# Performance work log

Measured on AMD Instinct MI355X. Metric: run time of the kernel, lower is better.

The kernel has to match this reference:

```python
import jax, jax.numpy as jnp
import numpy as np

PH, PW = 7, 7          # pooled output size (fixed by offset shape in module)
SPP = 2                # sample_per_part: bilinear samples per bin edge
SS = 0.0625            # spatial_scale = 1/16
TRANS_STD = 0.1


def setup_inputs() -> dict:
    key = jax.random.key(0)
    k1, k2, k3, k4, k5 = jax.random.split(key, 5)
    B, C, H, W = 8, 256, 168, 168
    N = 512
    img = W / SS  # input-image extent = 2688
    features = jax.random.normal(k1, (B, C, H, W), dtype=jnp.float32)
    bidx = jax.random.randint(k2, (N,), 0, B).astype(jnp.float32)
    xs = jnp.sort(jax.random.uniform(k3, (N, 2), minval=0.0, maxval=img - 1.0), axis=1)
    ys = jnp.sort(jax.random.uniform(k4, (N, 2), minval=0.0, maxval=img - 1.0), axis=1)
    rois = jnp.stack([bidx, xs[:, 0], ys[:, 0],
                      jnp.minimum(xs[:, 1] + 16.0, img - 1.0),
                      jnp.minimum(ys[:, 1] + 16.0, img - 1.0)], axis=1)
    offset = jax.random.normal(k5, (N, 2, PH, PW), dtype=jnp.float32)
    return {"features": features, "rois": rois, "offset": offset}


def _deform_roi_pool(features, rois, offset):
    B, C, H, W = features.shape
    off = offset * TRANS_STD  # module scales offsets by trans_std
    bidx = jax.lax.stop_gradient(rois[:, 0]).astype(jnp.int32)
    x1, y1, x2, y2 = rois[:, 1], rois[:, 2], rois[:, 3], rois[:, 4]
    # DCN kernel ROI geometry (0.5-pixel aligned, min size 0.1)
    sw = x1 * SS - 0.5
    sh = y1 * SS - 0.5
    rw = jnp.maximum((x2 + 1.0) * SS - 0.5 - sw, 0.1)
    rh = jnp.maximum((y2 + 1.0) * SS - 0.5 - sh, 0.1)
    bin_w, bin_h = rw / PW, rh / PH
    sub_w, sub_h = bin_w / SPP, bin_h / SPP

    e5 = lambda v: v[:, None, None, None, None]  # [N] -> [N,1,1,1,1]
    pw = jnp.arange(PW, dtype=features.dtype).reshape(1, 1, PW, 1, 1)
    ph = jnp.arange(PH, dtype=features.dtype).reshape(1, PH, 1, 1, 1)
    iw = (jnp.arange(SPP, dtype=features.dtype) + 0.5).reshape(1, 1, 1, 1, SPP)
    ih = (jnp.arange(SPP, dtype=features.dtype) + 0.5).reshape(1, 1, 1, SPP, 1)
    offx = off[:, 0][:, :, :, None, None]  # [N,PH,PW,1,1]
    offy = off[:, 1][:, :, :, None, None]

    # sample coords [N,PH,PW,SPP,SPP]: bin start + per-bin learned shift + sub-sample
    x = e5(sw) + pw * e5(bin_w) + offx * e5(rw) + iw * e5(sub_w)
    y = e5(sh) + ph * e5(bin_h) + offy * e5(rh) + ih * e5(sub_h)

    valid = (x > -0.5) & (x < W - 0.5) & (y > -0.5) & (y < H - 0.5)
    xc = jnp.clip(x, 0.0, W - 1.0)
    yc = jnp.clip(y, 0.0, H - 1.0)
    x0f, y0f = jnp.floor(xc), jnp.floor(yc)
    lx, ly = xc - x0f, yc - y0f
    x0 = x0f.astype(jnp.int32)
    y0 = y0f.astype(jnp.int32)
    x1i = jnp.minimum(x0 + 1, W - 1)
    y1i = jnp.minimum(y0 + 1, H - 1)

    # flat gather over (batch, h, w), channels vectorized
    featf = jnp.transpose(features, (0, 2, 3, 1)).reshape(B * H * W, C)
    base = e5(bidx) * (H * W)
    g = lambda yy, xx: featf[base + yy * W + xx]  # [N,PH,PW,SPP,SPP,C]

    w00 = ((1 - ly) * (1 - lx))[..., None]
    w01 = ((1 - ly) * lx)[..., None]
    w10 = (ly * (1 - lx))[..., None]
    w11 = (ly * lx)[..., None]
    val = w00 * g(y0, x0) + w01 * g(y0, x1i) + w10 * g(y1i, x0) + w11 * g(y1i, x1i)
    val = jnp.where(valid[..., None], val, 0.0)

    s = val.sum(axis=(3, 4))                                   # [N,PH,PW,C]
    cnt = valid.sum(axis=(3, 4)).astype(features.dtype)[..., None]
    out = jnp.where(cnt > 0, s / jnp.maximum(cnt, 1.0), 0.0)
    return jnp.transpose(out, (0, 3, 1, 2))                    # [N,C,PH,PW]


def reference(features, rois, offset):
    return _deform_roi_pool(features, rois, offset)
```

## Files before the change

kernel.cpp:

```cpp
#include <hip/hip_runtime.h>
#include <hip/hip_fp16.h>


#define PH_ 7
#define PW_ 7
#define SPP_ 2
#define SS_ 0.0625f
#define TRANS_STD_ 0.1f
#define B_ 8
#define C_ 256
#define H_ 168
#define W_ 168
#define N_ 512
#define HW_ (H_ * W_)
#define HW4_ (HW_ / 4)
#define BINS_ (PH_ * PW_)
#define NSUB_ (SPP_ * SPP_)
#define BLK_ 1024
#define RPC_ 20

#define WS_LIST_OFF_  B_
#define WS_DESC_OFF_I (B_ + B_ * N_)
#define DESC_FLOATS_  (N_ * NSUB_ * BINS_ * 4)
#define WS_NEEDED_    ((size_t)(WS_DESC_OFF_I) * 4 + (size_t)DESC_FLOATS_ * 4)

__global__ __launch_bounds__(512) void build_roi_lists(
    const float* __restrict__ rois, int* __restrict__ ws)
{
    const int r = threadIdx.x;
    if (r < B_) ws[r] = 0;
    __syncthreads();
    const int b = (int)rois[r * 5 + 0];
    const int pos = atomicAdd(&ws[b], 1);
    ws[WS_LIST_OFF_ + b * N_ + pos] = r;
}

__global__ __launch_bounds__(64) void build_desc(
    const float* __restrict__ rois,
    const float* __restrict__ offset,
    float4* __restrict__ desc)
{
    const int r   = blockIdx.x;
    const int bin = threadIdx.x;
    if (bin >= BINS_) return;
    const int ph = bin / PW_;
    const int pw = bin - ph * PW_;

    const float x1r = rois[r * 5 + 1];
    const float y1r = rois[r * 5 + 2];
    const float x2r = rois[r * 5 + 3];
    const float y2r = rois[r * 5 + 4];

    const float sw    = x1r * SS_ - 0.5f;
    const float sh    = y1r * SS_ - 0.5f;
    const float rw    = fmaxf((x2r + 1.0f) * SS_ - 0.5f - sw, 0.1f);
    const float rh    = fmaxf((y2r + 1.0f) * SS_ - 0.5f - sh, 0.1f);
    const float bin_w = rw * (1.0f / PW_);
    const float bin_h = rh * (1.0f / PH_);
    const float sub_w = bin_w * (1.0f / SPP_);
    const float sub_h = bin_h * (1.0f / SPP_);

    const float offx = offset[((r * 2 + 0) * PH_ + ph) * PW_ + pw] * TRANS_STD_;
    const float offy = offset[((r * 2 + 1) * PH_ + ph) * PW_ + pw] * TRANS_STD_;

    const float bx = sw + (float)pw * bin_w + offx * rw;
    const float by = sh + (float)ph * bin_h + offy * rh;

    unsigned pack[NSUB_];
    float lxs[NSUB_], lys[NSUB_];
    int   vals[NSUB_];
    int   cnt = 0;
#pragma unroll
    for (int s = 0; s < NSUB_; ++s) {
        const int ihs = s >> 1;
        const int iws = s & 1;
        const float x = bx + ((float)iws + 0.5f) * sub_w;
        const float y = by + ((float)ihs + 0.5f) * sub_h;
        const int valid = (x > -0.5f) && (x < (float)W_ - 0.5f) &&
                          (y > -0.5f) && (y < (float)H_ - 0.5f);
        const float xc = fminf(fmaxf(x, 0.0f), (float)(W_ - 1));
        const float yc = fminf(fmaxf(y, 0.0f), (float)(H_ - 1));
        const float x0f = floorf(xc);
        const float y0f = floorf(yc);
        const int x0 = (int)x0f;
        const int y0 = (int)y0f;
        const int dx = (x0 + 1 <= W_ - 1) ? 1 : 0;
        const int dy = (y0 + 1 <= H_ - 1) ? 1 : 0;
        pack[s] = (unsigned)(y0 * W_ + x0) | ((unsigned)dx << 15) |
                  ((unsigned)dy << 16);
        lxs[s] = xc - x0f;
        lys[s] = yc - y0f;
        vals[s] = valid;
        cnt += valid;
    }
    const float inv = (cnt > 0) ? (1.0f / (float)cnt) : 0.0f;
#pragma unroll
    for (int s = 0; s < NSUB_; ++s) {
        float4 d;
        d.x = __uint_as_float(pack[s]);
        d.y = lxs[s];
        d.z = lys[s];
        d.w = vals[s] ? inv : 0.0f;
        desc[((size_t)r * NSUB_ + s) * BINS_ + bin] = d;
    }
}

__global__ __launch_bounds__(BLK_, 8) void droi_pool_lds(
    const float* __restrict__ features,
    float* __restrict__ out,
    const int* __restrict__ ws)
{
    __shared__ __half plane[HW_];

    const int c   = blockIdx.x;
    const int b   = blockIdx.y;
    const int tid = threadIdx.x;

    const float4* __restrict__ f4 =
        reinterpret_cast<const float4*>(features + (size_t)(b * C_ + c) * HW_);
    for (int i = tid; i < HW4_; i += BLK_) {
        const float4 v = f4[i];
        union { __half2 h[2]; float2 f2; } u;
        u.h[0].x = __float2half(v.x); u.h[0].y = __float2half(v.y);
        u.h[1].x = __float2half(v.z); u.h[1].y = __float2half(v.w);
        *reinterpret_cast<float2*>(&plane[i * 4]) = u.f2;
    }
    __syncthreads();

    const int cnt_b = ws[b];
    const int* __restrict__ list = ws + WS_LIST_OFF_ + b * N_;
    const float4* __restrict__ desc =
        reinterpret_cast<const float4*>(ws + WS_DESC_OFF_I);

    const int q   = tid / BINS_;
    const int bin = tid - q * BINS_;
    const bool lane_ok = (q < RPC_);

    for (int base = 0; base < cnt_b; base += RPC_) {
        const int idx     = base + q;
        const bool active = lane_ok && (idx < cnt_b);
        const int r = list[active ? idx : 0];

        float acc = 0.0f;
#pragma unroll
        for (int s = 0; s < NSUB_; ++s) {
            const float4 d = desc[((size_t)r * NSUB_ + s) * BINS_ + bin];
            const unsigned pk = __float_as_uint(d.x);
            const int a00 = (int)(pk & 0x7FFFu);
            const int dx  = (int)((pk >> 15) & 1u);
            const int a10 = a00 + (int)((pk >> 16) & 1u) * W_;
            const float lx = d.y;
            const float ly = d.z;

            const float f00 = __half2float(plane[a00]);
            const float f01 = __half2float(plane[a00 + dx]);
            const float f10 = __half2float(plane[a10]);
            const float f11 = __half2float(plane[a10 + dx]);

            const float top = f00 + lx * (f01 - f00);
            const float bot = f10 + lx * (f11 - f10);
            acc += d.w * (top + ly * (bot - top));
        }

        if (active) {
            out[((size_t)r * C_ + c) * BINS_ + bin] = acc;
        }
    }
}

__global__ __launch_bounds__(64) void droi_pool_fallback(
    const float* __restrict__ features,
    const float* __restrict__ rois,
    const float* __restrict__ offset,
    float* __restrict__ out)
{
    const int blk  = blockIdx.x;
    const int n    = blk >> 8;
    const int c    = blk & 255;
    const int lane = threadIdx.x;
    if (lane >= BINS_) return;
    const int ph = lane / PW_;
    const int pw = lane % PW_;

    const float r0  = rois[n * 5 + 0];
    const float x1r = rois[n * 5 + 1];
    const float y1r = rois[n * 5 + 2];
    const float x2r = rois[n * 5 + 3];
    const float y2r = rois[n * 5 + 4];
    const int   b   = (int)r0;

    const float sw    = x1r * SS_ - 0.5f;
    const float sh    = y1r * SS_ - 0.5f;
    const float rw    = fmaxf((x2r + 1.0f) * SS_ - 0.5f - sw, 0.1f);
    const float rh    = fmaxf((y2r + 1.0f) * SS_ - 0.5f - sh, 0.1f);
    const float bin_w = rw / PW_;
    const float bin_h = rh / PH_;
    const float sub_w = bin_w / SPP_;
    const float sub_h = bin_h / SPP_;

    const float offx = offset[((n * 2 + 0) * PH_ + ph) * PW_ + pw] * TRANS_STD_;
    const float offy = offset[((n * 2 + 1) * PH_ + ph) * PW_ + pw] * TRANS_STD_;

    const float bx = sw + (float)pw * bin_w + offx * rw;
    const float by = sh + (float)ph * bin_h + offy * rh;

    const float* __restrict__ f =
        features + (size_t)(b * C_ + c) * (size_t)HW_;

    float s = 0.0f;
    int cnt = 0;
#pragma unroll
    for (int ihs = 0; ihs < SPP_; ++ihs) {
#pragma unroll
        for (int iws = 0; iws < SPP_; ++iws) {
            const float x = bx + ((float)iws + 0.5f) * sub_w;
            const float y = by + ((float)ihs + 0.5f) * sub_h;
            const bool valid = (x > -0.5f) && (x < (float)W_ - 0.5f) &&
                               (y > -0.5f) && (y < (float)H_ - 0.5f);
            const float xc = fminf(fmaxf(x, 0.0f), (float)(W_ - 1));
            const float yc = fminf(fmaxf(y, 0.0f), (float)(H_ - 1));
            const float x0f = floorf(xc);
            const float y0f = floorf(yc);
            const float lx = xc - x0f;
            const float ly = yc - y0f;
            const int x0 = (int)x0f;
            const int y0 = (int)y0f;
            const int x1i = min(x0 + 1, W_ - 1);
            const int y1i = min(y0 + 1, H_ - 1);
            const float f00 = f[y0  * W_ + x0 ];
            const float f01 = f[y0  * W_ + x1i];
            const float f10 = f[y1i * W_ + x0 ];
            const float f11 = f[y1i * W_ + x1i];
            const float v = (1.0f - ly) * (1.0f - lx) * f00 +
                            (1.0f - ly) * lx          * f01 +
                            ly          * (1.0f - lx) * f10 +
                            ly          * lx          * f11;
            if (valid) { s += v; cnt += 1; }
        }
    }
    const float res = (cnt > 0) ? (s / (float)cnt) : 0.0f;
    out[(size_t)(n * C_ + c) * BINS_ + lane] = res;
}

extern "C" void kernel_launch(void* const* d_in, const int* in_sizes, int n_in,
                              void* d_out, int out_size, void* d_ws, size_t ws_size,
                              hipStream_t stream) {
    const float* features = (const float*)d_in[0];
    const float* rois     = (const float*)d_in[1];
    const float* offset   = (const float*)d_in[2];
    float*       out      = (float*)d_out;

    if (ws_size >= WS_NEEDED_) {
        int* ws = (int*)d_ws;
        float4* desc = reinterpret_cast<float4*>(ws + WS_DESC_OFF_I);
        hipLaunchKernelGGL(build_roi_lists, dim3(1), dim3(N_), 0, stream,
                           rois, ws);
        hipLaunchKernelGGL(build_desc, dim3(N_), dim3(64), 0, stream,
                           rois, offset, desc);
        hipLaunchKernelGGL(droi_pool_lds, dim3(C_, B_), dim3(BLK_), 0, stream,
                           features, out, ws);
    } else {
        hipLaunchKernelGGL(droi_pool_fallback, dim3(N_ * C_), dim3(64), 0, stream,
                           features, rois, offset, out);
    }
}
```

Measured before the change: 346.0 us.

## Transpose features to channel-last fp16 pairs and sample per ROI from global memory

Replaces the per-(channel,batch) LDS plane kernel with two stages. A tiled transpose first writes features as HWC half2 channel pairs into workspace. A per-ROI kernel then gathers the bilinear corners directly from global memory with coalesced channel vectors and stages the outputs in LDS for contiguous float4 stores. This removes the ROI list build and the repeated full-plane LDS loads per channel. In exchange it adds a full-tensor transpose pass (about 231 MB read, 116 MB written) plus a larger workspace, and it relies on the cache to serve the scattered gathers.

Measured after the change: 363.0 us. 1.05x slower.

```diff
diff --git a/kernel.cpp b/kernel.cpp
--- a/kernel.cpp
+++ b/kernel.cpp
@@ -13,26 +13,49 @@
 #define W_ 168
 #define N_ 512
 #define HW_ (H_ * W_)
-#define HW4_ (HW_ / 4)
 #define BINS_ (PH_ * PW_)
 #define NSUB_ (SPP_ * SPP_)
-#define BLK_ 1024
-#define RPC_ 20
-
-#define WS_LIST_OFF_  B_
-#define WS_DESC_OFF_I (B_ + B_ * N_)
-#define DESC_FLOATS_  (N_ * NSUB_ * BINS_ * 4)
-#define WS_NEEDED_    ((size_t)(WS_DESC_OFF_I) * 4 + (size_t)DESC_FLOATS_ * 4)
-
-__global__ __launch_bounds__(512) void build_roi_lists(
-    const float* __restrict__ rois, int* __restrict__ ws)
-{
-    const int r = threadIdx.x;
-    if (r < B_) ws[r] = 0;
+#define CP_ (C_ / 2)
+
+#define T_BYTES_   ((size_t)B_ * HW_ * CP_ * 4)
+#define DESC_BYTES_ ((size_t)N_ * NSUB_ * BINS_ * 16)
+#define WS_NEEDED_ (T_BYTES_ + DESC_BYTES_)
+
+__global__ __launch_bounds__(256) void transpose_pairs(
+    const float* __restrict__ features, __half2* __restrict__ T)
+{
+    __shared__ float tile[64][65];
+    const int pblk = blockIdx.x;
+    const int cblk = blockIdx.y;
+    const int b    = blockIdx.z;
+    const int tid  = threadIdx.x;
+
+    {
+        const int p_l    = tid & 63;
+        const int c_base = tid >> 6;
+        const size_t gbase =
+            ((size_t)(b * C_ + cblk * 64) ) * HW_ + (size_t)pblk * 64 + p_l;
+#pragma unroll 4
+        for (int j = 0; j < 16; ++j) {
+            const int c_l = j * 4 + c_base;
+            tile[c_l][p_l] = features[gbase + (size_t)c_l * HW_];
+        }
+    }
     __syncthreads();
-    const int b = (int)rois[r * 5 + 0];
-    const int pos = atomicAdd(&ws[b], 1);
-    ws[WS_LIST_OFF_ + b * N_ + pos] = r;
+
+    {
+        const int cp_l   = tid & 31;
+        const int p_base = tid >> 5;
+#pragma unroll 4
+        for (int j = 0; j < 8; ++j) {
+            const int p_l = j * 8 + p_base;
+            const __half2 h = __halves2half2(
+                __float2half(tile[2 * cp_l][p_l]),
+                __float2half(tile[2 * cp_l + 1][p_l]));
+            T[((size_t)b * HW_ + (size_t)pblk * 64 + p_l) * CP_
+              + cblk * 32 + cp_l] = h;
+        }
+    }
 }
 
 __global__ __launch_bounds__(64) void build_desc(
@@ -105,67 +128,61 @@
     }
 }
 
-__global__ __launch_bounds__(BLK_, 8) void droi_pool_lds(
-    const float* __restrict__ features,
-    float* __restrict__ out,
-    const int* __restrict__ ws)
-{
-    __shared__ __half plane[HW_];
-
-    const int c   = blockIdx.x;
-    const int b   = blockIdx.y;
+__global__ __launch_bounds__(512) void droi_sample(
+    const __half2* __restrict__ T,
+    const float* __restrict__ rois,
+    const float4* __restrict__ desc,
+    float* __restrict__ out)
+{
+    __shared__ float tile[C_ * BINS_];
+
+    const int r   = blockIdx.x;
     const int tid = threadIdx.x;
-
-    const float4* __restrict__ f4 =
-        reinterpret_cast<const float4*>(features + (size_t)(b * C_ + c) * HW_);
-    for (int i = tid; i < HW4_; i += BLK_) {
-        const float4 v = f4[i];
-        union { __half2 h[2]; float2 f2; } u;
-        u.h[0].x = __float2half(v.x); u.h[0].y = __float2half(v.y);
-        u.h[1].x = __float2half(v.z); u.h[1].y = __float2half(v.w);
-        *reinterpret_cast<float2*>(&plane[i * 4]) = u.f2;
+    const int bg  = tid >> 7;
+    const int cp  = tid & 127;
+    const int b   = (int)rois[r * 5];
+
+    const __half2* __restrict__ Tb = T + (size_t)b * HW_ * CP_ + cp;
+
+    for (int bin = bg; bin < BINS_; bin += 4) {
+        const int bin_u = __builtin_amdgcn_readfirstlane(bin);
+        float acc0 = 0.0f, acc1 = 0.0f;
+#pragma unroll
+        for (int s = 0; s < NSUB_; ++s) {
+            const float4 d = desc[((size_t)r * NSUB_ + s) * BINS_ + bin_u];
+            const unsigned pk = __float_as_uint(d.x);
+            const int p00 = (int)(pk & 0x7FFFu);
+            const int dx  = (int)((pk >> 15) & 1u);
+            const int dyW = (int)((pk >> 16) & 1u) * W_;
+            const float lx = d.y, ly = d.z, sc = d.w;
+
+            const __half2 h00 = Tb[(size_t)p00 * CP_];
+            const __half2 h01 = Tb[(size_t)(p00 + dx) * CP_];
+            const __half2 h10 = Tb[(size_t)(p00 + dyW) * CP_];
+            const __half2 h11 = Tb[(size_t)(p00 + dyW + dx) * CP_];
+
+            const float f00x = __low2float(h00), f00y = __high2float(h00);
+            const float f01x = __low2float(h01), f01y = __high2float(h01);
+            const float f10x = __low2float(h10), f10y = __high2float(h10);
+            const float f11x = __low2float(h11), f11y = __high2float(h11);
+
+            const float tx = f00x + lx * (f01x - f00x);
+            const float bxv = f10x + lx * (f11x - f10x);
+            acc0 += sc * (tx + ly * (bxv - tx));
+
+            const float ty = f00y + lx * (f01y - f00y);
+            const float byv = f10y + lx * (f11y - f10y);
+            acc1 += sc * (ty + ly * (byv - ty));
+        }
+        tile[(2 * cp) * BINS_ + bin_u]     = acc0;
+        tile[(2 * cp + 1) * BINS_ + bin_u] = acc1;
     }
     __syncthreads();
 
-    const int cnt_b = ws[b];
-    const int* __restrict__ list = ws + WS_LIST_OFF_ + b * N_;
-    const float4* __restrict__ desc =
-        reinterpret_cast<const float4*>(ws + WS_DESC_OFF_I);
-
-    const int q   = tid / BINS_;
-    const int bin = tid - q * BINS_;
-    const bool lane_ok = (q < RPC_);
-
-    for (int base = 0; base < cnt_b; base += RPC_) {
-        const int idx     = base + q;
-        const bool active = lane_ok && (idx < cnt_b);
-        const int r = list[active ? idx : 0];
-
-        float acc = 0.0f;
-#pragma unroll
-        for (int s = 0; s < NSUB_; ++s) {
-            const float4 d = desc[((size_t)r * NSUB_ + s) * BINS_ + bin];
-            const unsigned pk = __float_as_uint(d.x);
-            const int a00 = (int)(pk & 0x7FFFu);
-            const int dx  = (int)((pk >> 15) & 1u);
-            const int a10 = a00 + (int)((pk >> 16) & 1u) * W_;
-            const float lx = d.y;
-            const float ly = d.z;
-
-            const float f00 = __half2float(plane[a00]);
-            const float f01 = __half2float(plane[a00 + dx]);
-            const float f10 = __half2float(plane[a10]);
-            const float f11 = __half2float(plane[a10 + dx]);
-
-            const float top = f00 + lx * (f01 - f00);
-            const float bot = f10 + lx * (f11 - f10);
-            acc += d.w * (top + ly * (bot - top));
-        }
-
-        if (active) {
-            out[((size_t)r * C_ + c) * BINS_ + bin] = acc;
-        }
-    }
+    const float4* __restrict__ t4 = reinterpret_cast<const float4*>(tile);
+    float4* __restrict__ o4 =
+        reinterpret_cast<float4*>(out + (size_t)r * (C_ * BINS_));
+    for (int k = tid; k < (C_ * BINS_) / 4; k += 512) o4[k] = t4[k];
 }
 
 __global__ __launch_bounds__(64) void droi_pool_fallback(
@@ -251,14 +268,14 @@
     float*       out      = (float*)d_out;
 
     if (ws_size >= WS_NEEDED_) {
-        int* ws = (int*)d_ws;
-        float4* desc = reinterpret_cast<float4*>(ws + WS_DESC_OFF_I);
-        hipLaunchKernelGGL(build_roi_lists, dim3(1), dim3(N_), 0, stream,
-                           rois, ws);
+        __half2* T   = reinterpret_cast<__half2*>(d_ws);
+        float4* desc = reinterpret_cast<float4*>((char*)d_ws + T_BYTES_);
+        hipLaunchKernelGGL(transpose_pairs, dim3(HW_ / 64, C_ / 64, B_),
+                           dim3(256), 0, stream, features, T);
         hipLaunchKernelGGL(build_desc, dim3(N_), dim3(64), 0, stream,
                            rois, offset, desc);
-        hipLaunchKernelGGL(droi_pool_lds, dim3(C_, B_), dim3(BLK_), 0, stream,
-                           features, out, ws);
+        hipLaunchKernelGGL(droi_sample, dim3(N_), dim3(512), 0, stream,
+                           T, rois, desc, out);
     } else {
         hipLaunchKernelGGL(droi_pool_fallback, dim3(N_ * C_), dim3(64), 0, stream,
                            features, rois, offset, out);
```
